# Performance work log

Hardware: AMD Instinct MI355X
Metric: run time of the kernel (lower is better)

## Reference

```python
import jax, jax.numpy as jnp
import numpy as np

N_NODES = 100000
N_EDGES = 600000
IN_SIZE = 128
OUT_SIZE = 128
N_GRAPHS = 100
BN_EPS = 1e-5


def setup_inputs() -> dict:
    key = jax.random.key(0)
    ks = jax.random.split(key, 8)
    h = jax.random.normal(ks[0], (N_NODES, IN_SIZE), dtype=jnp.float32)
    norm = jax.random.uniform(ks[1], (N_NODES, 1), dtype=jnp.float32)
    src = jax.random.randint(ks[2], (N_EDGES,), 0, N_NODES, dtype=jnp.int32)
    dst = jax.random.randint(ks[3], (N_EDGES,), 0, N_NODES, dtype=jnp.int32)
    graph_ids = jnp.sort(jax.random.randint(ks[4], (N_NODES,), 0, N_GRAPHS, dtype=jnp.int32))
    # Linear + BatchNorm params
    W = jax.random.normal(ks[5], (IN_SIZE, OUT_SIZE), dtype=jnp.float32) / np.sqrt(IN_SIZE)
    b = jnp.zeros((OUT_SIZE,), dtype=jnp.float32)
    gamma = jnp.ones((OUT_SIZE,), dtype=jnp.float32)
    beta = jnp.zeros((OUT_SIZE,), dtype=jnp.float32)
    return {"h": h, "norm": norm, "W": W, "b": b, "gamma": gamma, "beta": beta,
            "src": src, "dst": dst, "graph_ids": graph_ids}


def reference(h, norm, W, b, gamma, beta, src, dst, graph_ids):
    # pre-normalize, scatter-sum over edges (copy_src + sum), post-normalize
    x = h * norm                                            # [N, in]
    agg = jax.ops.segment_sum(x[src], dst, num_segments=N_NODES)  # SpMM
    x = agg * norm
    # linear + relu
    x = jax.nn.relu(jnp.dot(x, W) + b)                      # [N, out]
    # BatchNorm1d (training-mode: batch mean, biased variance)
    mean = jnp.mean(x, axis=0)
    var = jnp.mean(jnp.square(x - mean), axis=0)
    x = (x - mean) * jax.lax.rsqrt(var + BN_EPS) * gamma + beta
    # sum_nodes pooling per graph
    phis = jax.ops.segment_sum(x, graph_ids, num_segments=N_GRAPHS)  # [G, out]
    return (x, phis)
```

## Files before the change

### kernel.cpp

```cpp
#include <hip/hip_runtime.h>
#include <hip/hip_bf16.h>

#define N_NODES 100000
#define N_PAD 100096
#define N_EDGES 600000
#define CH 128
#define N_GRAPHS 100
#define BN_EPS 1e-5f
#define NBUCKET 64
#define CAP 16
#define OVFCAP 8192
#define FILL_BLOCKS 586
#define GEMM_BLOCKS 782
#define GATHER_BLOCKS 1024
#define ZERO_INTS (N_NODES + 2 * NBUCKET * CH + 4)
#define ZERO_BLOCKS 455

typedef __bf16 bf16x8 __attribute__((ext_vector_type(8)));
typedef float f32x4 __attribute__((ext_vector_type(4)));

__device__ __forceinline__ ushort f2bf(float f) {
    union { float f; unsigned u; } x; x.f = f;
    unsigned u = x.u;
    unsigned r = (u + 0x7fffu + ((u >> 16) & 1u)) >> 16;
    return (ushort)r;
}
__device__ __forceinline__ float bflo(unsigned p) { return __builtin_bit_cast(float, p << 16); }
__device__ __forceinline__ float bfhi(unsigned p) { return __builtin_bit_cast(float, p & 0xffff0000u); }

__global__ __launch_bounds__(256) void k_prep(const float* __restrict__ W,
        int* __restrict__ zbase, ushort* __restrict__ Wt) {
    unsigned bid = blockIdx.x;
    if (bid < ZERO_BLOCKS) {
        int i = bid * 256 + threadIdx.x;
        if (i < ZERO_INTS) zbase[i] = 0;
    } else {
        int t = (bid - ZERO_BLOCKS) * 256 + threadIdx.x;
        int k = t >> 7, o = t & 127;
        Wt[o * CH + k] = f2bf(W[t]);
    }
}

__device__ __forceinline__ bf16x8 mk_a(const float* __restrict__ hrow, int k,
                                       float nm, bool valid) {
    union { bf16x8 v; ushort u[8]; } r;
    if (valid) {
        float4 p = *(const float4*)(hrow + k);
        float4 q = *(const float4*)(hrow + k + 4);
        r.u[0] = f2bf(p.x * nm); r.u[1] = f2bf(p.y * nm);
        r.u[2] = f2bf(p.z * nm); r.u[3] = f2bf(p.w * nm);
        r.u[4] = f2bf(q.x * nm); r.u[5] = f2bf(q.y * nm);
        r.u[6] = f2bf(q.z * nm); r.u[7] = f2bf(q.w * nm);
    } else {
        #pragma unroll
        for (int i = 0; i < 8; i++) r.u[i] = 0;
    }
    return r.v;
}

__global__ __launch_bounds__(256) void k_front(const int* __restrict__ src,
        const int* __restrict__ dst, const float* __restrict__ h,
        const float* __restrict__ norm, const ushort* __restrict__ Wt,
        int* __restrict__ cnt, int* __restrict__ ovfcur, int* __restrict__ ovf,
        int* __restrict__ esrc, ushort* __restrict__ z16) {
    __shared__ ushort ys[128 * CH];
    unsigned bid = blockIdx.x;
    int tid = threadIdx.x;

    if (bid < FILL_BLOCKS) {
        int e0 = (bid * 256 + tid) * 4;
        if (e0 < N_EDGES) {
            int4 d = *(const int4*)(dst + e0);
            int4 s = *(const int4*)(src + e0);
            int s0 = atomicAdd(&cnt[d.x], 1);
            int s1 = atomicAdd(&cnt[d.y], 1);
            int s2 = atomicAdd(&cnt[d.z], 1);
            int s3 = atomicAdd(&cnt[d.w], 1);
            if (s0 < CAP) esrc[d.x * CAP + s0] = s.x;
            else { int p = atomicAdd(ovfcur, 1); if (p < OVFCAP) { ovf[2*p] = d.x; ovf[2*p+1] = s.x; } }
            if (s1 < CAP) esrc[d.y * CAP + s1] = s.y;
            else { int p = atomicAdd(ovfcur, 1); if (p < OVFCAP) { ovf[2*p] = d.y; ovf[2*p+1] = s.y; } }
            if (s2 < CAP) esrc[d.z * CAP + s2] = s.z;
            else { int p = atomicAdd(ovfcur, 1); if (p < OVFCAP) { ovf[2*p] = d.z; ovf[2*p+1] = s.z; } }
            if (s3 < CAP) esrc[d.w * CAP + s3] = s.w;
            else { int p = atomicAdd(ovfcur, 1); if (p < OVFCAP) { ovf[2*p] = d.w; ovf[2*p+1] = s.w; } }
        }
        return;
    }

    int gb = bid - FILL_BLOCKS;
    int w = tid >> 6, L = tid & 63;
    int c15 = L & 15, quad = L >> 4;
    int nb = gb * 128 + w * 32;
    int r0 = nb + c15, r1 = nb + 16 + c15;
    bool v0r = r0 < N_NODES, v1r = r1 < N_NODES;
    float nm0 = v0r ? norm[r0] : 0.f;
    float nm1 = v1r ? norm[r1] : 0.f;
    const float* h0 = h + (size_t)r0 * CH;
    const float* h1 = h + (size_t)r1 * CH;

    f32x4 acc0[8] = {}, acc1[8] = {};
    #pragma unroll
    for (int kt = 0; kt < 4; kt++) {
        int k = kt * 32 + quad * 8;
        bf16x8 a0 = mk_a(h0, k, nm0, v0r);
        bf16x8 a1 = mk_a(h1, k, nm1, v1r);
        #pragma unroll
        for (int ot = 0; ot < 8; ot++) {
            bf16x8 b = *(const bf16x8*)(Wt + (size_t)(ot * 16 + c15) * CH + k);
            acc0[ot] = __builtin_amdgcn_mfma_f32_16x16x32_bf16(a0, b, acc0[ot], 0, 0, 0);
            acc1[ot] = __builtin_amdgcn_mfma_f32_16x16x32_bf16(a1, b, acc1[ot], 0, 0, 0);
        }
    }

    #pragma unroll
    for (int ot = 0; ot < 8; ot++) {
        int col = ot * 16 + c15;
        #pragma unroll
        for (int r = 0; r < 4; r++) {
            ys[(w * 32 + quad * 4 + r) * CH + col] = f2bf(acc0[ot][r]);
            ys[(w * 32 + 16 + quad * 4 + r) * CH + col] = f2bf(acc1[ot][r]);
        }
    }
    __syncthreads();
    {
        const uint4* ysv = (const uint4*)ys;
        uint4* out = (uint4*)(z16 + (size_t)gb * 128 * CH);
        #pragma unroll
        for (int i = 0; i < 8; i++) out[tid + i * 256] = ysv[tid + i * 256];
    }
}

__global__ __launch_bounds__(256) void k_gather(const ushort* __restrict__ z16,
        const float* __restrict__ norm, const int* __restrict__ cnt,
        const int* __restrict__ esrc, const int* __restrict__ ovfcur,
        const int* __restrict__ ovf, const float* __restrict__ bias,
        ushort* __restrict__ y16, float* __restrict__ psum, float* __restrict__ psq) {
    __shared__ float sred[2][16][CH];

    int tid = threadIdx.x;
    int cg = tid & 15, rl = tid >> 4;
    int c = cg * 8;
    float4 b0 = *(const float4*)(bias + c), b1 = *(const float4*)(bias + c + 4);
    float s8[8] = {}, q8[8] = {};
    int no = min(*ovfcur, OVFCAP);

    for (int n = blockIdx.x * 16 + rl; n < N_NODES; n += GATHER_BLOCKS * 16) {
        int e = min(cnt[n], CAP);
        float nn = norm[n];
        int base = n * CAP;
        float a0=0.f,a1=0.f,a2=0.f,a3=0.f,a4=0.f,a5=0.f,a6=0.f,a7=0.f;
        int j = 0;
        for (; j + 4 <= e; j += 4) {
            int4 s4 = *(const int4*)(esrc + base + j);
            uint4 v0 = *(const uint4*)(z16 + (size_t)s4.x * CH + c);
            uint4 v1 = *(const uint4*)(z16 + (size_t)s4.y * CH + c);
            uint4 v2 = *(const uint4*)(z16 + (size_t)s4.z * CH + c);
            uint4 v3 = *(const uint4*)(z16 + (size_t)s4.w * CH + c);
            a0 += bflo(v0.x) + bflo(v1.x) + bflo(v2.x) + bflo(v3.x);
            a1 += bfhi(v0.x) + bfhi(v1.x) + bfhi(v2.x) + bfhi(v3.x);
            a2 += bflo(v0.y) + bflo(v1.y) + bflo(v2.y) + bflo(v3.y);
            a3 += bfhi(v0.y) + bfhi(v1.y) + bfhi(v2.y) + bfhi(v3.y);
            a4 += bflo(v0.z) + bflo(v1.z) + bflo(v2.z) + bflo(v3.z);
            a5 += bfhi(v0.z) + bfhi(v1.z) + bfhi(v2.z) + bfhi(v3.z);
            a6 += bflo(v0.w) + bflo(v1.w) + bflo(v2.w) + bflo(v3.w);
            a7 += bfhi(v0.w) + bfhi(v1.w) + bfhi(v2.w) + bfhi(v3.w);
        }
        for (; j < e; j++) {
            int s = esrc[base + j];
            uint4 v = *(const uint4*)(z16 + (size_t)s * CH + c);
            a0 += bflo(v.x); a1 += bfhi(v.x);
            a2 += bflo(v.y); a3 += bfhi(v.y);
            a4 += bflo(v.z); a5 += bfhi(v.z);
            a6 += bflo(v.w); a7 += bfhi(v.w);
        }
        if (no > 0) {
            for (int i = 0; i < no; i++) {
                if (ovf[2*i] == n) {
                    int s = ovf[2*i+1];
                    uint4 v = *(const uint4*)(z16 + (size_t)s * CH + c);
                    a0 += bflo(v.x); a1 += bfhi(v.x);
                    a2 += bflo(v.y); a3 += bfhi(v.y);
                    a4 += bflo(v.z); a5 += bfhi(v.z);
                    a6 += bflo(v.w); a7 += bfhi(v.w);
                }
            }
        }
        float f[8];
        f[0] = fmaxf(fmaf(a0, nn, b0.x), 0.f);
        f[1] = fmaxf(fmaf(a1, nn, b0.y), 0.f);
        f[2] = fmaxf(fmaf(a2, nn, b0.z), 0.f);
        f[3] = fmaxf(fmaf(a3, nn, b0.w), 0.f);
        f[4] = fmaxf(fmaf(a4, nn, b1.x), 0.f);
        f[5] = fmaxf(fmaf(a5, nn, b1.y), 0.f);
        f[6] = fmaxf(fmaf(a6, nn, b1.z), 0.f);
        f[7] = fmaxf(fmaf(a7, nn, b1.w), 0.f);
        uint4 o;
        o.x = (unsigned)f2bf(f[0]) | ((unsigned)f2bf(f[1]) << 16);
        o.y = (unsigned)f2bf(f[2]) | ((unsigned)f2bf(f[3]) << 16);
        o.z = (unsigned)f2bf(f[4]) | ((unsigned)f2bf(f[5]) << 16);
        o.w = (unsigned)f2bf(f[6]) | ((unsigned)f2bf(f[7]) << 16);
        *(uint4*)(y16 + (size_t)n * CH + c) = o;
        #pragma unroll
        for (int k = 0; k < 8; k++) { s8[k] += f[k]; q8[k] += f[k] * f[k]; }
    }

    *(float4*)&sred[0][rl][c]     = make_float4(s8[0], s8[1], s8[2], s8[3]);
    *(float4*)&sred[0][rl][c + 4] = make_float4(s8[4], s8[5], s8[6], s8[7]);
    *(float4*)&sred[1][rl][c]     = make_float4(q8[0], q8[1], q8[2], q8[3]);
    *(float4*)&sred[1][rl][c + 4] = make_float4(q8[4], q8[5], q8[6], q8[7]);
    __syncthreads();
    if (tid < 128) {
        float S = 0.f, Q = 0.f;
        #pragma unroll
        for (int k = 0; k < 16; k++) { S += sred[0][k][tid]; Q += sred[1][k][tid]; }
        int bucket = blockIdx.x & (NBUCKET - 1);
        atomicAdd(&psum[bucket * CH + tid], S);
        atomicAdd(&psq[bucket * CH + tid], Q);
    }
}

__global__ void k_finalize(const float* __restrict__ psum, const float* __restrict__ psq,
        const float* __restrict__ gamma, const float* __restrict__ beta,
        float* __restrict__ scale, float* __restrict__ shift, float* __restrict__ phis) {
    int t = threadIdx.x;
    float S = 0.f, Q = 0.f;
    for (int g = 0; g < NBUCKET; g++) { S += psum[g * CH + t]; Q += psq[g * CH + t]; }
    const float invN = 1.f / (float)N_NODES;
    float mean = S * invN;
    float var  = Q * invN - mean * mean;
    float sc   = gamma[t] * rsqrtf(var + BN_EPS);
    scale[t] = sc;
    shift[t] = beta[t] - mean * sc;
    for (int i = t; i < N_GRAPHS * CH; i += 128) phis[i] = 0.f;
}

__global__ __launch_bounds__(256) void k_bnpool(const ushort* __restrict__ y16,
        const int* __restrict__ gids, const float* __restrict__ scale,
        const float* __restrict__ shift, float* __restrict__ xout,
        float* __restrict__ phis) {
    __shared__ float smP[16][CH];

    int tid = threadIdx.x;
    int cg = tid & 15, rl = tid >> 4;
    int c = cg * 8;
    int r0 = blockIdx.x * 256;
    int rbase = r0 + rl * 16;

    float4 sc0 = *(const float4*)(scale + c), sc1 = *(const float4*)(scale + c + 4);
    float4 sh0 = *(const float4*)(shift + c), sh1 = *(const float4*)(shift + c + 4);

    bool fast = (r0 + 255 < N_NODES) && (gids[r0] == gids[r0 + 255]);

    if (fast) {
        float4 p0 = make_float4(0.f,0.f,0.f,0.f), p1 = make_float4(0.f,0.f,0.f,0.f);
        for (int j = 0; j < 16; j++) {
            int r = rbase + j;
            uint4 v = *(const uint4*)(y16 + (size_t)r * CH + c);
            float4 f0, f1;
            f0.x = fmaf(bflo(v.x), sc0.x, sh0.x); f0.y = fmaf(bfhi(v.x), sc0.y, sh0.y);
            f0.z = fmaf(bflo(v.y), sc0.z, sh0.z); f0.w = fmaf(bfhi(v.y), sc0.w, sh0.w);
            f1.x = fmaf(bflo(v.z), sc1.x, sh1.x); f1.y = fmaf(bfhi(v.z), sc1.y, sh1.y);
            f1.z = fmaf(bflo(v.w), sc1.z, sh1.z); f1.w = fmaf(bfhi(v.w), sc1.w, sh1.w);
            *(float4*)(xout + (size_t)r * CH + c) = f0;
            *(float4*)(xout + (size_t)r * CH + c + 4) = f1;
            p0.x += f0.x; p0.y += f0.y; p0.z += f0.z; p0.w += f0.w;
            p1.x += f1.x; p1.y += f1.y; p1.z += f1.z; p1.w += f1.w;
        }
        *(float4*)&smP[rl][c] = p0;
        *(float4*)&smP[rl][c + 4] = p1;
        __syncthreads();
        if (tid < 128) {
            int g = gids[r0];
            float S = 0.f;
            #pragma unroll
            for (int k = 0; k < 16; k++) S += smP[k][tid];
            atomicAdd(&phis[(size_t)g * CH + tid], S);
        }
    } else {
        float p[8] = {};
        int gprev = -1;
        for (int j = 0; j < 16; j++) {
            int r = rbase + j;
            if (r >= N_NODES) break;
            int g = gids[r];
            if (g != gprev) {
                if (gprev >= 0) {
                    #pragma unroll
                    for (int k = 0; k < 8; k++) {
                        atomicAdd(&phis[(size_t)gprev * CH + c + k], p[k]);
                        p[k] = 0.f;
                    }
                }
                gprev = g;
            }
            uint4 v = *(const uint4*)(y16 + (size_t)r * CH + c);
            float f[8];
            f[0] = fmaf(bflo(v.x), sc0.x, sh0.x); f[1] = fmaf(bfhi(v.x), sc0.y, sh0.y);
            f[2] = fmaf(bflo(v.y), sc0.z, sh0.z); f[3] = fmaf(bfhi(v.y), sc0.w, sh0.w);
            f[4] = fmaf(bflo(v.z), sc1.x, sh1.x); f[5] = fmaf(bfhi(v.z), sc1.y, sh1.y);
            f[6] = fmaf(bflo(v.w), sc1.z, sh1.z); f[7] = fmaf(bfhi(v.w), sc1.w, sh1.w);
            *(float4*)(xout + (size_t)r * CH + c) = make_float4(f[0], f[1], f[2], f[3]);
            *(float4*)(xout + (size_t)r * CH + c + 4) = make_float4(f[4], f[5], f[6], f[7]);
            #pragma unroll
            for (int k = 0; k < 8; k++) p[k] += f[k];
        }
        if (gprev >= 0) {
            #pragma unroll
            for (int k = 0; k < 8; k++)
                atomicAdd(&phis[(size_t)gprev * CH + c + k], p[k]);
        }
    }
}

extern "C" void kernel_launch(void* const* d_in, const int* in_sizes, int n_in,
                              void* d_out, int out_size, void* d_ws, size_t ws_size,
                              hipStream_t stream)
{
    const float* h     = (const float*)d_in[0];
    const float* norm  = (const float*)d_in[1];
    const float* W     = (const float*)d_in[2];
    const float* b     = (const float*)d_in[3];
    const float* gamma = (const float*)d_in[4];
    const float* beta  = (const float*)d_in[5];
    const int*   src   = (const int*)d_in[6];
    const int*   dst   = (const int*)d_in[7];
    const int*   gids  = (const int*)d_in[8];

    float* x_out = (float*)d_out;
    float* phis  = x_out + (size_t)N_NODES * CH;

    ushort* z16  = (ushort*)d_ws;
    ushort* y16  = z16 + (size_t)N_PAD * CH;
    ushort* Wt   = y16 + (size_t)N_PAD * CH;
    int*   cnt     = (int*)(Wt + CH * CH);
    float* psum    = (float*)(cnt + N_NODES);
    float* psq     = psum + NBUCKET * CH;
    int*   ovfcur  = (int*)(psq + NBUCKET * CH);
    int*   esrc    = ovfcur + 4;
    int*   ovf     = esrc + (size_t)N_NODES * CAP;
    float* scale   = (float*)(ovf + 2 * OVFCAP);
    float* shift   = scale + CH;

    k_prep<<<ZERO_BLOCKS + 64, 256, 0, stream>>>(W, cnt, Wt);
    k_front<<<FILL_BLOCKS + GEMM_BLOCKS, 256, 0, stream>>>(
        src, dst, h, norm, Wt, cnt, ovfcur, ovf, esrc, z16);
    k_gather<<<GATHER_BLOCKS, 256, 0, stream>>>(
        z16, norm, cnt, esrc, ovfcur, ovf, b, y16, psum, psq);
    k_finalize<<<1, 128, 0, stream>>>(psum, psq, gamma, beta, scale, shift, phis);
    k_bnpool<<<(N_NODES + 255) / 256, 256, 0, stream>>>(y16, gids, scale, shift, x_out, phis);
}
```

Before: 229.6 us.

## Fold BN finalize into bnpool, swap MFMA operands to store GEMM output directly

Removes the single-block k_finalize launch: each k_bnpool block now recomputes BN scale and shift from the partial sums in shared memory, and zeroing of phis moves into k_prep. The GEMM swaps its A and B operands so each lane holds contiguous output columns of one node and writes them to global memory directly, dropping the 32KB shared-memory staging buffer and its barrier. Reduces the stat buckets from 64 to 16, which makes the per-block recompute cheaper but concentrates more atomics on each bucket. Removes padding from the workspace layout.

```diff
diff --git a/kernel.cpp b/kernel.cpp
--- a/kernel.cpp
+++ b/kernel.cpp
@@ -2,19 +2,20 @@
 #include <hip/hip_bf16.h>
 
 #define N_NODES 100000
-#define N_PAD 100096
 #define N_EDGES 600000
 #define CH 128
 #define N_GRAPHS 100
 #define BN_EPS 1e-5f
-#define NBUCKET 64
+#define NBUCKET 16
 #define CAP 16
 #define OVFCAP 8192
 #define FILL_BLOCKS 586
 #define GEMM_BLOCKS 782
 #define GATHER_BLOCKS 1024
 #define ZERO_INTS (N_NODES + 2 * NBUCKET * CH + 4)
-#define ZERO_BLOCKS 455
+#define ZERO_BLOCKS 407
+#define PHIS_BLOCKS 50
+#define WT_BLOCKS 64
 
 typedef __bf16 bf16x8 __attribute__((ext_vector_type(8)));
 typedef float f32x4 __attribute__((ext_vector_type(4)));
@@ -29,19 +30,23 @@
 __device__ __forceinline__ float bfhi(unsigned p) { return __builtin_bit_cast(float, p & 0xffff0000u); }
 
 __global__ __launch_bounds__(256) void k_prep(const float* __restrict__ W,
-        int* __restrict__ zbase, ushort* __restrict__ Wt) {
+        int* __restrict__ zbase, ushort* __restrict__ Wt, float* __restrict__ phis) {
     unsigned bid = blockIdx.x;
+    int tid = threadIdx.x;
     if (bid < ZERO_BLOCKS) {
-        int i = bid * 256 + threadIdx.x;
+        int i = bid * 256 + tid;
         if (i < ZERO_INTS) zbase[i] = 0;
+    } else if (bid < ZERO_BLOCKS + PHIS_BLOCKS) {
+        int i = (bid - ZERO_BLOCKS) * 256 + tid;
+        phis[i] = 0.f;
     } else {
-        int t = (bid - ZERO_BLOCKS) * 256 + threadIdx.x;
+        int t = (bid - ZERO_BLOCKS - PHIS_BLOCKS) * 256 + tid;
         int k = t >> 7, o = t & 127;
         Wt[o * CH + k] = f2bf(W[t]);
     }
 }
 
-__device__ __forceinline__ bf16x8 mk_a(const float* __restrict__ hrow, int k,
+__device__ __forceinline__ bf16x8 mk_b(const float* __restrict__ hrow, int k,
                                        float nm, bool valid) {
     union { bf16x8 v; ushort u[8]; } r;
     if (valid) {
@@ -63,7 +68,6 @@
         const float* __restrict__ norm, const ushort* __restrict__ Wt,
         int* __restrict__ cnt, int* __restrict__ ovfcur, int* __restrict__ ovf,
         int* __restrict__ esrc, ushort* __restrict__ z16) {
-    __shared__ ushort ys[128 * CH];
     unsigned bid = blockIdx.x;
     int tid = threadIdx.x;
 
@@ -92,42 +96,46 @@
     int w = tid >> 6, L = tid & 63;
     int c15 = L & 15, quad = L >> 4;
     int nb = gb * 128 + w * 32;
-    int r0 = nb + c15, r1 = nb + 16 + c15;
-    bool v0r = r0 < N_NODES, v1r = r1 < N_NODES;
-    float nm0 = v0r ? norm[r0] : 0.f;
-    float nm1 = v1r ? norm[r1] : 0.f;
-    const float* h0 = h + (size_t)r0 * CH;
-    const float* h1 = h + (size_t)r1 * CH;
+    int n0 = nb + c15, n1 = nb + 16 + c15;
+    bool v0 = n0 < N_NODES, v1 = n1 < N_NODES;
+    float nm0 = v0 ? norm[n0] : 0.f;
+    float nm1 = v1 ? norm[n1] : 0.f;
+    const float* h0 = h + (size_t)n0 * CH;
+    const float* h1 = h + (size_t)n1 * CH;
 
     f32x4 acc0[8] = {}, acc1[8] = {};
     #pragma unroll
     for (int kt = 0; kt < 4; kt++) {
         int k = kt * 32 + quad * 8;
-        bf16x8 a0 = mk_a(h0, k, nm0, v0r);
-        bf16x8 a1 = mk_a(h1, k, nm1, v1r);
+        bf16x8 b0 = mk_b(h0, k, nm0, v0);
+        bf16x8 b1 = mk_b(h1, k, nm1, v1);
         #pragma unroll
         for (int ot = 0; ot < 8; ot++) {
-            bf16x8 b = *(const bf16x8*)(Wt + (size_t)(ot * 16 + c15) * CH + k);
-            acc0[ot] = __builtin_amdgcn_mfma_f32_16x16x32_bf16(a0, b, acc0[ot], 0, 0, 0);
-            acc1[ot] = __builtin_amdgcn_mfma_f32_16x16x32_bf16(a1, b, acc1[ot], 0, 0, 0);
-        }
-    }
-
-    #pragma unroll
-    for (int ot = 0; ot < 8; ot++) {
-        int col = ot * 16 + c15;
-        #pragma unroll
-        for (int r = 0; r < 4; r++) {
-            ys[(w * 32 + quad * 4 + r) * CH + col] = f2bf(acc0[ot][r]);
-            ys[(w * 32 + 16 + quad * 4 + r) * CH + col] = f2bf(acc1[ot][r]);
-        }
-    }
-    __syncthreads();
-    {
-        const uint4* ysv = (const uint4*)ys;
-        uint4* out = (uint4*)(z16 + (size_t)gb * 128 * CH);
-        #pragma unroll
-        for (int i = 0; i < 8; i++) out[tid + i * 256] = ysv[tid + i * 256];
+            bf16x8 a = *(const bf16x8*)(Wt + (size_t)(ot * 16 + c15) * CH + k);
+            acc0[ot] = __builtin_amdgcn_mfma_f32_16x16x32_bf16(a, b0, acc0[ot], 0, 0, 0);
+            acc1[ot] = __builtin_amdgcn_mfma_f32_16x16x32_bf16(a, b1, acc1[ot], 0, 0, 0);
+        }
+    }
+
+    if (v0) {
+        ushort* zr = z16 + (size_t)n0 * CH;
+        #pragma unroll
+        for (int ot = 0; ot < 8; ot++) {
+            uint2 dv;
+            dv.x = (unsigned)f2bf(acc0[ot][0]) | ((unsigned)f2bf(acc0[ot][1]) << 16);
+            dv.y = (unsigned)f2bf(acc0[ot][2]) | ((unsigned)f2bf(acc0[ot][3]) << 16);
+            *(uint2*)(zr + ot * 16 + quad * 4) = dv;
+        }
+    }
+    if (v1) {
+        ushort* zr = z16 + (size_t)n1 * CH;
+        #pragma unroll
+        for (int ot = 0; ot < 8; ot++) {
+            uint2 dv;
+            dv.x = (unsigned)f2bf(acc1[ot][0]) | ((unsigned)f2bf(acc1[ot][1]) << 16);
+            dv.y = (unsigned)f2bf(acc1[ot][2]) | ((unsigned)f2bf(acc1[ot][3]) << 16);
+            *(uint2*)(zr + ot * 16 + quad * 4) = dv;
+        }
     }
 }
 
@@ -220,35 +228,35 @@
     }
 }
 
-__global__ void k_finalize(const float* __restrict__ psum, const float* __restrict__ psq,
-        const float* __restrict__ gamma, const float* __restrict__ beta,
-        float* __restrict__ scale, float* __restrict__ shift, float* __restrict__ phis) {
-    int t = threadIdx.x;
-    float S = 0.f, Q = 0.f;
-    for (int g = 0; g < NBUCKET; g++) { S += psum[g * CH + t]; Q += psq[g * CH + t]; }
-    const float invN = 1.f / (float)N_NODES;
-    float mean = S * invN;
-    float var  = Q * invN - mean * mean;
-    float sc   = gamma[t] * rsqrtf(var + BN_EPS);
-    scale[t] = sc;
-    shift[t] = beta[t] - mean * sc;
-    for (int i = t; i < N_GRAPHS * CH; i += 128) phis[i] = 0.f;
-}
-
 __global__ __launch_bounds__(256) void k_bnpool(const ushort* __restrict__ y16,
-        const int* __restrict__ gids, const float* __restrict__ scale,
-        const float* __restrict__ shift, float* __restrict__ xout,
+        const int* __restrict__ gids, const float* __restrict__ psum,
+        const float* __restrict__ psq, const float* __restrict__ gamma,
+        const float* __restrict__ beta, float* __restrict__ xout,
         float* __restrict__ phis) {
     __shared__ float smP[16][CH];
+    __shared__ float ssc[CH], ssh[CH];
 
     int tid = threadIdx.x;
+    if (tid < 128) {
+        float S = 0.f, Q = 0.f;
+        #pragma unroll
+        for (int g = 0; g < NBUCKET; g++) { S += psum[g * CH + tid]; Q += psq[g * CH + tid]; }
+        const float invN = 1.f / (float)N_NODES;
+        float mean = S * invN;
+        float var  = Q * invN - mean * mean;
+        float sc   = gamma[tid] * rsqrtf(var + BN_EPS);
+        ssc[tid] = sc;
+        ssh[tid] = beta[tid] - mean * sc;
+    }
+    __syncthreads();
+
     int cg = tid & 15, rl = tid >> 4;
     int c = cg * 8;
     int r0 = blockIdx.x * 256;
     int rbase = r0 + rl * 16;
 
-    float4 sc0 = *(const float4*)(scale + c), sc1 = *(const float4*)(scale + c + 4);
-    float4 sh0 = *(const float4*)(shift + c), sh1 = *(const float4*)(shift + c + 4);
+    float4 sc0 = *(const float4*)&ssc[c], sc1 = *(const float4*)&ssc[c + 4];
+    float4 sh0 = *(const float4*)&ssh[c], sh1 = *(const float4*)&ssh[c + 4];
 
     bool fast = (r0 + 255 < N_NODES) && (gids[r0] == gids[r0 + 255]);
 
@@ -331,22 +339,20 @@
     float* phis  = x_out + (size_t)N_NODES * CH;
 
     ushort* z16  = (ushort*)d_ws;
-    ushort* y16  = z16 + (size_t)N_PAD * CH;
-    ushort* Wt   = y16 + (size_t)N_PAD * CH;
+    ushort* y16  = z16 + (size_t)N_NODES * CH;
+    ushort* Wt   = y16 + (size_t)N_NODES * CH;
     int*   cnt     = (int*)(Wt + CH * CH);
     float* psum    = (float*)(cnt + N_NODES);
     float* psq     = psum + NBUCKET * CH;
     int*   ovfcur  = (int*)(psq + NBUCKET * CH);
     int*   esrc    = ovfcur + 4;
     int*   ovf     = esrc + (size_t)N_NODES * CAP;
-    float* scale   = (float*)(ovf + 2 * OVFCAP);
-    float* shift   = scale + CH;
-
-    k_prep<<<ZERO_BLOCKS + 64, 256, 0, stream>>>(W, cnt, Wt);
+
+    k_prep<<<ZERO_BLOCKS + PHIS_BLOCKS + WT_BLOCKS, 256, 0, stream>>>(W, cnt, Wt, phis);
     k_front<<<FILL_BLOCKS + GEMM_BLOCKS, 256, 0, stream>>>(
         src, dst, h, norm, Wt, cnt, ovfcur, ovf, esrc, z16);
     k_gather<<<GATHER_BLOCKS, 256, 0, stream>>>(
         z16, norm, cnt, esrc, ovfcur, ovf, b, y16, psum, psq);
-    k_finalize<<<1, 128, 0, stream>>>(psum, psq, gamma, beta, scale, shift, phis);
-    k_bnpool<<<(N_NODES + 255) / 256, 256, 0, stream>>>(y16, gids, scale, shift, x_out, phis);
-}
+    k_bnpool<<<(N_NODES + 255) / 256, 256, 0, stream>>>(
+        y16, gids, psum, psq, gamma, beta, x_out, phis);
+}
```

Result: no change. 230.9 us (+0.6%).
